# Performance work log

Measured on AMD Instinct MI355X. Metric: run time of the kernel, lower is better.

Reference implementation:

```python
import jax, jax.numpy as jnp
jax.config.update("jax_enable_x64", True)
import numpy as np
import math

N = 100_000   # number of events
D = 4         # feature dim
M = 256       # number of Gaussian centers
E = 10        # ensemble size
SIGMA = 0.1
NORM_CONST = 1.0 / ((2.0 * math.pi) ** (D / 2) * SIGMA ** D)


def setup_inputs() -> dict:
    key = jax.random.key(0)
    k = jax.random.split(key, 6)
    x = jax.random.normal(k[0], (N, D), dtype=jnp.float64)
    centers = jax.random.normal(k[1], (M, D), dtype=jnp.float64)
    coefficients = jax.random.normal(k[2], (M,), dtype=jnp.float64)
    ensemble_probs = jax.random.uniform(k[3], (N, E), dtype=jnp.float64)
    ensemble_norm_probs = jax.random.uniform(k[4], (N, 1), dtype=jnp.float64)
    # small positive weights so 1 - sum(w) stays positive (as in a fitted model)
    weights = 0.05 * jax.random.uniform(k[5], (E,), dtype=jnp.float64)
    return {
        "x": x,
        "ensemble_probs": ensemble_probs,
        "ensemble_norm_probs": ensemble_norm_probs,
        "weights": weights,
        "centers": centers,
        "coefficients": coefficients,
    }


def reference(x, ensemble_probs, ensemble_norm_probs, weights, centers, coefficients):
    # GaussianKernelLayer.get_kernels: pairwise squared distances -> RBF
    diff = x[:, None, :] - centers[None, :, :]          # [N, M, D]
    dist_sq = jnp.sum(diff * diff, axis=2)              # [N, M]
    kern = NORM_CONST * jnp.exp(-0.5 * dist_sq / (SIGMA ** 2))  # [N, M]
    # centered coefficients, contract: einsum('m,Nm->N')
    wc = coefficients - coefficients.mean()
    net_out = kern @ wc                                 # [N]
    # ensemble mixture: w [E,1], w_norm [1,1]
    w = weights[:, None]
    w_norm = 1.0 - jnp.sum(w, axis=0, keepdims=True)
    ensemble = ensemble_probs @ w + ensemble_norm_probs @ w_norm  # [N, 1]
    return (ensemble, net_out)
```

## Files before the change

### kernel.cpp

```cpp
#include <hip/hip_runtime.h>
#include <math.h>

#define NROWS 100000
#define MCENT 256
#define EENS 10

#define NORM_CONST_F 253.30295910584444f
#define EXP2_SCALE (-72.13475204444817f)

__global__ __launch_bounds__(256) void fused_kernel(
    const float* __restrict__ x,
    const float* __restrict__ ensemble_probs,
    const float* __restrict__ ensemble_norm_probs,
    const float* __restrict__ weights,
    const float* __restrict__ centers,
    const float* __restrict__ coefficients,
    float* __restrict__ out)
{
    __shared__ float s_p1[4][64];
    __shared__ float s_p2[4][64];

    const int t = threadIdx.x;
    const int lane = t & 63;
    const int wid = __builtin_amdgcn_readfirstlane(t >> 6);

    const int r = blockIdx.x * 64 + lane;
    const int rc = (r < NROWS) ? r : (NROWS - 1);

    const float4 xv = ((const float4*)x)[rc];

    const float4* __restrict__ C = (const float4*)centers + wid * 64;
    const float*  __restrict__ K = coefficients + wid * 64;

    float a1_0 = 0.f, a1_1 = 0.f;
    float a2_0 = 0.f, a2_1 = 0.f;

    #pragma unroll 8
    for (int k = 0; k < 64; k += 2) {
        {
            const float4 c = C[k];
            const float cf = K[k];
            const float dx = xv.x - c.x, dy = xv.y - c.y,
                        dz = xv.z - c.z, dw = xv.w - c.w;
            float d2 = dx * dx;
            d2 = fmaf(dy, dy, d2);
            d2 = fmaf(dz, dz, d2);
            d2 = fmaf(dw, dw, d2);
            const float e = __builtin_amdgcn_exp2f(d2 * EXP2_SCALE);
            a1_0 = fmaf(cf, e, a1_0);
            a2_0 += e;
        }
        {
            const float4 c = C[k + 1];
            const float cf = K[k + 1];
            const float dx = xv.x - c.x, dy = xv.y - c.y,
                        dz = xv.z - c.z, dw = xv.w - c.w;
            float d2 = dx * dx;
            d2 = fmaf(dy, dy, d2);
            d2 = fmaf(dz, dz, d2);
            d2 = fmaf(dw, dw, d2);
            const float e = __builtin_amdgcn_exp2f(d2 * EXP2_SCALE);
            a1_1 = fmaf(cf, e, a1_1);
            a2_1 += e;
        }
    }

    s_p1[wid][lane] = a1_0 + a1_1;
    s_p2[wid][lane] = a2_0 + a2_1;
    __syncthreads();

    if (wid == 0) {
        const float4 cf4 = ((const float4*)coefficients)[lane];
        float s = (cf4.x + cf4.y) + (cf4.z + cf4.w);
        #pragma unroll
        for (int off = 32; off > 0; off >>= 1) s += __shfl_down(s, off, 64);
        const float mean = __builtin_amdgcn_readfirstlane(s) * (1.0f / 256.0f);

        if (r < NROWS) {
            const float P1 = (s_p1[0][lane] + s_p1[1][lane]) +
                             (s_p1[2][lane] + s_p1[3][lane]);
            const float P2 = (s_p2[0][lane] + s_p2[1][lane]) +
                             (s_p2[2][lane] + s_p2[3][lane]);
            out[NROWS + r] = (P1 - mean * P2) * NORM_CONST_F;
        }
    } else if (wid == 1) {
        if (r < NROWS) {
            float wv[EENS];
            float wsum = 0.0f;
            #pragma unroll
            for (int e = 0; e < EENS; ++e) { wv[e] = weights[e]; wsum += wv[e]; }
            float ens = ensemble_norm_probs[r] * (1.0f - wsum);
            const float2* pr = (const float2*)(ensemble_probs + (size_t)r * EENS);
            #pragma unroll
            for (int e2 = 0; e2 < EENS / 2; ++e2) {
                const float2 p = pr[e2];
                ens = fmaf(p.x, wv[2 * e2 + 0], ens);
                ens = fmaf(p.y, wv[2 * e2 + 1], ens);
            }
            out[r] = ens;
        }
    }
}

extern "C" void kernel_launch(void* const* d_in, const int* in_sizes, int n_in,
                              void* d_out, int out_size, void* d_ws, size_t ws_size,
                              hipStream_t stream) {
    const float* x       = (const float*)d_in[0];
    const float* eprobs  = (const float*)d_in[1];
    const float* enorm   = (const float*)d_in[2];
    const float* weights = (const float*)d_in[3];
    const float* centers = (const float*)d_in[4];
    const float* coeffs  = (const float*)d_in[5];
    float* out = (float*)d_out;

    const int blocks = (NROWS + 63) / 64;
    fused_kernel<<<blocks, 256, 0, stream>>>(
        x, eprobs, enorm, weights, centers, coeffs, out);
}
```

Baseline: 15.35 us.

## Split centers across 8 waves, pre-center coefficients, prefetch ensemble loads early

Each 64-row block now uses 512 threads, so each of 8 waves handles 32 centers instead of 4 waves handling 64. This shortens the serial loop per wave. Every wave computes the coefficient mean up front and subtracts it per center, which drops the second accumulator and the P2 reduction. The ensemble-probability loads are issued before the kernel loop so their latency overlaps the compute. In exchange, the mean reduction is repeated in every wave and the larger blocks can hurt occupancy and scheduling.

```diff
diff --git a/kernel.cpp b/kernel.cpp
--- a/kernel.cpp
+++ b/kernel.cpp
@@ -4,11 +4,12 @@
 #define NROWS 100000
 #define MCENT 256
 #define EENS 10
+#define WAVES 8
 
 #define NORM_CONST_F 253.30295910584444f
 #define EXP2_SCALE (-72.13475204444817f)
 
-__global__ __launch_bounds__(256) void fused_kernel(
+__global__ __launch_bounds__(512) void fused_kernel(
     const float* __restrict__ x,
     const float* __restrict__ ensemble_probs,
     const float* __restrict__ ensemble_norm_probs,
@@ -17,8 +18,7 @@
     const float* __restrict__ coefficients,
     float* __restrict__ out)
 {
-    __shared__ float s_p1[4][64];
-    __shared__ float s_p2[4][64];
+    __shared__ float s_p[WAVES][64];
 
     const int t = threadIdx.x;
     const int lane = t & 63;
@@ -29,59 +29,59 @@
 
     const float4 xv = ((const float4*)x)[rc];
 
-    const float4* __restrict__ C = (const float4*)centers + wid * 64;
-    const float*  __restrict__ K = coefficients + wid * 64;
+    float2 pr0, pr1, pr2, pr3, pr4;
+    float npv = 0.0f;
+    if (wid == 1) {
+        const float2* pr = (const float2*)(ensemble_probs + (size_t)rc * EENS);
+        pr0 = pr[0]; pr1 = pr[1]; pr2 = pr[2]; pr3 = pr[3]; pr4 = pr[4];
+        npv = ensemble_norm_probs[rc];
+    }
 
-    float a1_0 = 0.f, a1_1 = 0.f;
-    float a2_0 = 0.f, a2_1 = 0.f;
+    const float4 cf4 = ((const float4*)coefficients)[lane];
+    float s = (cf4.x + cf4.y) + (cf4.z + cf4.w);
+    #pragma unroll
+    for (int off = 32; off > 0; off >>= 1) s += __shfl_down(s, off, 64);
+    const float mean = __builtin_amdgcn_readfirstlane(s) * (1.0f / 256.0f);
 
+    const float4* __restrict__ C = (const float4*)centers + wid * 32;
+    const float*  __restrict__ K = coefficients + wid * 32;
+
+    float acc0 = 0.f, acc1 = 0.f;
     #pragma unroll 8
-    for (int k = 0; k < 64; k += 2) {
+    for (int k = 0; k < 32; k += 2) {
         {
             const float4 c = C[k];
-            const float cf = K[k];
+            const float wc = K[k] - mean;
             const float dx = xv.x - c.x, dy = xv.y - c.y,
                         dz = xv.z - c.z, dw = xv.w - c.w;
             float d2 = dx * dx;
             d2 = fmaf(dy, dy, d2);
             d2 = fmaf(dz, dz, d2);
             d2 = fmaf(dw, dw, d2);
-            const float e = __builtin_amdgcn_exp2f(d2 * EXP2_SCALE);
-            a1_0 = fmaf(cf, e, a1_0);
-            a2_0 += e;
+            acc0 = fmaf(wc, __builtin_amdgcn_exp2f(d2 * EXP2_SCALE), acc0);
         }
         {
             const float4 c = C[k + 1];
-            const float cf = K[k + 1];
+            const float wc = K[k + 1] - mean;
             const float dx = xv.x - c.x, dy = xv.y - c.y,
                         dz = xv.z - c.z, dw = xv.w - c.w;
             float d2 = dx * dx;
             d2 = fmaf(dy, dy, d2);
             d2 = fmaf(dz, dz, d2);
             d2 = fmaf(dw, dw, d2);
-            const float e = __builtin_amdgcn_exp2f(d2 * EXP2_SCALE);
-            a1_1 = fmaf(cf, e, a1_1);
-            a2_1 += e;
+            acc1 = fmaf(wc, __builtin_amdgcn_exp2f(d2 * EXP2_SCALE), acc1);
         }
     }
 
-    s_p1[wid][lane] = a1_0 + a1_1;
-    s_p2[wid][lane] = a2_0 + a2_1;
+    s_p[wid][lane] = acc0 + acc1;
     __syncthreads();
 
     if (wid == 0) {
-        const float4 cf4 = ((const float4*)coefficients)[lane];
-        float s = (cf4.x + cf4.y) + (cf4.z + cf4.w);
-        #pragma unroll
-        for (int off = 32; off > 0; off >>= 1) s += __shfl_down(s, off, 64);
-        const float mean = __builtin_amdgcn_readfirstlane(s) * (1.0f / 256.0f);
-
         if (r < NROWS) {
-            const float P1 = (s_p1[0][lane] + s_p1[1][lane]) +
-                             (s_p1[2][lane] + s_p1[3][lane]);
-            const float P2 = (s_p2[0][lane] + s_p2[1][lane]) +
-                             (s_p2[2][lane] + s_p2[3][lane]);
-            out[NROWS + r] = (P1 - mean * P2) * NORM_CONST_F;
+            float P = 0.f;
+            #pragma unroll
+            for (int w = 0; w < WAVES; ++w) P += s_p[w][lane];
+            out[NROWS + r] = P * NORM_CONST_F;
         }
     } else if (wid == 1) {
         if (r < NROWS) {
@@ -89,14 +89,17 @@
             float wsum = 0.0f;
             #pragma unroll
             for (int e = 0; e < EENS; ++e) { wv[e] = weights[e]; wsum += wv[e]; }
-            float ens = ensemble_norm_probs[r] * (1.0f - wsum);
-            const float2* pr = (const float2*)(ensemble_probs + (size_t)r * EENS);
-            #pragma unroll
-            for (int e2 = 0; e2 < EENS / 2; ++e2) {
-                const float2 p = pr[e2];
-                ens = fmaf(p.x, wv[2 * e2 + 0], ens);
-                ens = fmaf(p.y, wv[2 * e2 + 1], ens);
-            }
+            float ens = npv * (1.0f - wsum);
+            ens = fmaf(pr0.x, wv[0], ens);
+            ens = fmaf(pr0.y, wv[1], ens);
+            ens = fmaf(pr1.x, wv[2], ens);
+            ens = fmaf(pr1.y, wv[3], ens);
+            ens = fmaf(pr2.x, wv[4], ens);
+            ens = fmaf(pr2.y, wv[5], ens);
+            ens = fmaf(pr3.x, wv[6], ens);
+            ens = fmaf(pr3.y, wv[7], ens);
+            ens = fmaf(pr4.x, wv[8], ens);
+            ens = fmaf(pr4.y, wv[9], ens);
             out[r] = ens;
         }
     }
@@ -114,6 +117,6 @@
     float* out = (float*)d_out;
 
     const int blocks = (NROWS + 63) / 64;
-    fused_kernel<<<blocks, 256, 0, stream>>>(
+    fused_kernel<<<blocks, 512, 0, stream>>>(
         x, eprobs, enorm, weights, centers, coeffs, out);
 }
```

After: 15.60 us. No clear change (+1.7%).
